# Kernel optimization log

Hardware: AMD Instinct MI355X
Metric: run time of the kernel (lower is better)

Reference implementation:

```python
import jax, jax.numpy as jnp
import numpy as np
from jax import lax

B, S, D, F, E, K = 4, 2048, 2048, 8192, 8, 2


def setup_inputs() -> dict:
    key = jax.random.key(0)
    ks = jax.random.split(key, 4)
    sd = 1.0 / np.sqrt(D)
    sf = 1.0 / np.sqrt(F)
    return {
        "hidden_states": jax.random.normal(ks[0], (B, S, D), dtype=jnp.float32),
        "router_w": jax.random.normal(ks[1], (D, E), dtype=jnp.float32) * sd,
        "w1": jax.random.normal(ks[2], (E, D, F), dtype=jnp.float32) * sd,
        "b1": jnp.zeros((E, F), dtype=jnp.float32),
        "w2": jax.random.normal(ks[3], (E, F, D), dtype=jnp.float32) * sf,
        "b2": jnp.zeros((E, D), dtype=jnp.float32),
        "top_k": K,
    }


def reference(hidden_states, router_w, w1, b1, w2, b2, top_k):
    b, s, d = hidden_states.shape
    x = hidden_states.reshape(-1, d)  # [T, D] flat tokens
    # Router: top-k over expert logits, softmax over the selected logits.
    logits = x @ router_w                      # [T, E]
    top_vals, top_idx = lax.top_k(logits, top_k)  # [T, K]
    scores = jax.nn.softmax(top_vals, axis=-1)    # [T, K]

    out = jnp.zeros_like(x)
    n_experts = w1.shape[0]
    for e in range(n_experts):  # fixed small expert count
        # per-token combine weight for this expert (0 if not routed)
        cw = jnp.sum(jnp.where(top_idx == e, scores, 0.0), axis=-1)  # [T]
        h = jax.nn.gelu(x @ w1[e] + b1[e], approximate=False)        # [T, F]
        out = out + cw[:, None] * (h @ w2[e] + b2[e])                # masked combine
    out = out.reshape(b, s, d)
    return out + hidden_states  # use_residual=True
```

## Files before the change

kernel.cpp:

```cpp
#include <hip/hip_runtime.h>

#define T_TOK 8192
#define DIM   2048
#define FFN   8192
#define NE    8
#define TOPK  2

typedef unsigned short ushort_t;
typedef unsigned short ushort8  __attribute__((ext_vector_type(8)));
typedef unsigned short ushort4v __attribute__((ext_vector_type(4)));
typedef short bf16x8 __attribute__((ext_vector_type(8)));
typedef float f32x4  __attribute__((ext_vector_type(4)));

__device__ __forceinline__ ushort_t f2bf(float f) {
  unsigned int u = __float_as_uint(f);
  u += 0x7FFFu + ((u >> 16) & 1u);
  return (ushort_t)(u >> 16);
}
__device__ __forceinline__ float bf2f(ushort_t u) {
  return __uint_as_float(((unsigned int)u) << 16);
}

__device__ __forceinline__ void gload16(const void* g, void* l) {
  __builtin_amdgcn_global_load_lds((const __attribute__((address_space(1))) void*)g,
                                   (__attribute__((address_space(3))) void*)l, 16, 0, 0);
}
__device__ __forceinline__ unsigned lds_off(const ushort_t* p) {
  return (unsigned)(uintptr_t)(__attribute__((address_space(3))) const ushort_t*)p;
}
__device__ __forceinline__ bf16x8 ds_read128(unsigned off) {
  bf16x8 r;
  asm volatile("ds_read_b128 %0, %1" : "=v"(r) : "v"(off));
  return r;
}

__device__ __forceinline__ float gelu_exact(float v) {
  float s = v * 0.70710678118654752f;
  float a = fabsf(s);
  float t = __builtin_amdgcn_rcpf(1.0f + 0.3275911f * a);
  float p = t * (0.254829592f +
            t * (-0.284496736f +
            t * (1.421413741f +
            t * (-1.453152027f +
            t * 1.061405429f))));
  float er = 1.0f - p * __expf(-a * a);
  er = copysignf(er, s);
  return 0.5f * v * (1.0f + er);
}

__global__ void k_cast(const float* __restrict__ x, ushort_t* __restrict__ xbf) {
  int i = blockIdx.x * blockDim.x + threadIdx.x;
  float4 v = reinterpret_cast<const float4*>(x)[i];
  ushort4v o;
  o.x = f2bf(v.x); o.y = f2bf(v.y); o.z = f2bf(v.z); o.w = f2bf(v.w);
  reinterpret_cast<ushort4v*>(xbf)[i] = o;
}

#define TT 64
__global__ __launch_bounds__(256) void k_wcvt(const float* __restrict__ in,
                                              ushort_t* __restrict__ outp, int R, int C) {
  __shared__ ushort_t t[TT][TT + 8];
  int e = blockIdx.z;
  const float* src = in + (size_t)e * R * C;
  ushort_t* dst = outp + (size_t)e * R * C;
  int r0 = blockIdx.y * TT, c0 = blockIdx.x * TT;
  int tid = threadIdx.x;
  int rr = tid >> 4;
  int c4 = tid & 15;
#pragma unroll
  for (int i = 0; i < 4; i++) {
    int r = rr + i * 16;
    float4 v = *reinterpret_cast<const float4*>(src + (size_t)(r0 + r) * C + c0 + c4 * 4);
    ushort4v p;
    p.x = f2bf(v.x); p.y = f2bf(v.y); p.z = f2bf(v.z); p.w = f2bf(v.w);
    *reinterpret_cast<ushort4v*>(&t[r][c4 * 4]) = p;
  }
  __syncthreads();
  int c = tid >> 2, rs = tid & 3;
  ushort_t tmp[16];
#pragma unroll
  for (int i = 0; i < 16; i++) tmp[i] = t[rs * 16 + i][c];
  ushort8 v0, v1;
#pragma unroll
  for (int i = 0; i < 8; i++) { v0[i] = tmp[i]; v1[i] = tmp[8 + i]; }
  ushort_t* drow = dst + (size_t)(c0 + c) * R + r0 + rs * 16;
  *reinterpret_cast<ushort8*>(drow) = v0;
  *reinterpret_cast<ushort8*>(drow + 8) = v1;
}

__global__ __launch_bounds__(256) void k_router(
    const float* __restrict__ x, const float* __restrict__ rw,
    int* __restrict__ tidx, float* __restrict__ twt, int* __restrict__ counts) {
  int t = blockIdx.x;
  int tid = threadIdx.x;
  int lane = tid & 63, wave = tid >> 6;
  float acc[NE];
#pragma unroll
  for (int e = 0; e < NE; e++) acc[e] = 0.f;
  const float* xr = x + (size_t)t * DIM;
  for (int d = tid; d < DIM; d += 256) {
    float xv = xr[d];
    const float* r = rw + d * NE;
#pragma unroll
    for (int e = 0; e < NE; e++) acc[e] += xv * r[e];
  }
  __shared__ float wsum[4][NE];
#pragma unroll
  for (int e = 0; e < NE; e++) {
    float v = acc[e];
#pragma unroll
    for (int off = 32; off > 0; off >>= 1) v += __shfl_down(v, off);
    if (lane == 0) wsum[wave][e] = v;
  }
  __syncthreads();
  if (tid == 0) {
    float lg[NE];
#pragma unroll
    for (int e = 0; e < NE; e++) lg[e] = wsum[0][e] + wsum[1][e] + wsum[2][e] + wsum[3][e];
    int i0 = 0; float v0 = lg[0];
#pragma unroll
    for (int e = 1; e < NE; e++) if (lg[e] > v0) { v0 = lg[e]; i0 = e; }
    int i1 = -1; float v1 = -3.4e38f;
#pragma unroll
    for (int e = 0; e < NE; e++) if (e != i0 && lg[e] > v1) { v1 = lg[e]; i1 = e; }
    float e1 = expf(v1 - v0);
    float s = 1.f + e1;
    tidx[t * 2 + 0] = i0; tidx[t * 2 + 1] = i1;
    twt[t * 2 + 0] = 1.f / s; twt[t * 2 + 1] = e1 / s;
    atomicAdd(&counts[i0], 1);
    atomicAdd(&counts[i1], 1);
  }
}

__global__ void k_scan(const int* __restrict__ counts, int* __restrict__ offsets) {
  if (threadIdx.x == 0) {
    int s = 0;
    for (int e = 0; e < NE; e++) { offsets[e] = s; s += counts[e]; }
    offsets[NE] = s;
  }
}

__global__ void k_fill(const int* __restrict__ tidx, const float* __restrict__ twt,
                       const int* __restrict__ offsets, int* __restrict__ cursors,
                       int* __restrict__ ltok, float* __restrict__ lwt, int* __restrict__ ppos) {
  int t = blockIdx.x * blockDim.x + threadIdx.x;
  if (t >= T_TOK) return;
#pragma unroll
  for (int k = 0; k < TOPK; k++) {
    int e = tidx[t * 2 + k];
    int pos = atomicAdd(&cursors[e], 1);
    int p = offsets[e] + pos;
    ltok[p] = t;
    lwt[p] = twt[t * 2 + k];
    ppos[t * 2 + k] = p;
  }
}

#define BM 128
#define BN 128
#define BK 32
#define BUFB (BM * BK * 2)

__device__ __forceinline__ void xcd_decode(int lin, int nwg, int nx, int& xt, int& yt) {
  int q = nwg >> 3;
  int w = (lin & 7) * q + (lin >> 3);
  xt = w % nx;
  yt = w / nx;
}

template <int NT>
__device__ __forceinline__ void gemm_loop(const ushort_t* __restrict__ a0,
                                          const ushort_t* __restrict__ a1,
                                          const ushort_t* __restrict__ b0,
                                          const ushort_t* __restrict__ b1,
                                          ushort_t* AsLds, ushort_t* BsLds,
                                          f32x4 (&acc)[4][4]) {
  int tid = threadIdx.x;
  int wave = tid >> 6, lane = tid & 63;
  int wm = wave >> 1, wn = wave & 1;
  int lm = lane & 15, lg = lane >> 4;

  unsigned abase = lds_off(AsLds), bbase = lds_off(BsLds);
  unsigned aoff[4], boff[4];
#pragma unroll
  for (int m = 0; m < 4; m++)
    aoff[m] = abase + ((wm * 64 + m * 16 + lm) * BK + lg * 8) * 2;
#pragma unroll
  for (int n = 0; n < 4; n++)
    boff[n] = bbase + ((wn * 64 + n * 16 + lm) * BK + lg * 8) * 2;

  const ushort_t* ap[2] = {a0, a1};
  const ushort_t* bp[2] = {b0, b1};

  auto STAGE = [&](int buf, int k0) {
#pragma unroll
    for (int j = 0; j < 2; j++) {
      gload16(ap[j] + k0, AsLds + buf * (BM * BK) + (j * 256 + wave * 64) * 8);
      gload16(bp[j] + k0, BsLds + buf * (BM * BK) + (j * 256 + wave * 64) * 8);
    }
  };

  STAGE(0, 0);
  STAGE(1, BK);
  int cur = 0;
  for (int t = 0; t < NT; ++t) {
    int s2 = cur + 2; if (s2 >= 3) s2 -= 3;
    if (t + 2 < NT) {
      STAGE(s2, (t + 2) * BK);
      __builtin_amdgcn_sched_barrier(0);
      asm volatile("s_waitcnt vmcnt(8)" ::: "memory");
    } else if (t + 1 < NT) {
      __builtin_amdgcn_sched_barrier(0);
      asm volatile("s_waitcnt vmcnt(4)" ::: "memory");
    } else {
      __builtin_amdgcn_sched_barrier(0);
      asm volatile("s_waitcnt vmcnt(0)" ::: "memory");
    }
    __builtin_amdgcn_s_barrier();
    __builtin_amdgcn_sched_barrier(0);
    unsigned cb = (unsigned)(cur * BUFB);
    bf16x8 af[4], bv[4];
#pragma unroll
    for (int m = 0; m < 4; m++) af[m] = ds_read128(aoff[m] + cb);
#pragma unroll
    for (int n = 0; n < 4; n++) bv[n] = ds_read128(boff[n] + cb);
    asm volatile("s_waitcnt lgkmcnt(0)" ::: "memory");
    __builtin_amdgcn_sched_barrier(0);
#pragma unroll
    for (int m = 0; m < 4; m++)
#pragma unroll
      for (int n = 0; n < 4; n++)
        acc[m][n] = __builtin_amdgcn_mfma_f32_16x16x32_bf16(af[m], bv[n], acc[m][n], 0, 0, 0);
    __builtin_amdgcn_sched_barrier(0);
    __builtin_amdgcn_s_barrier();
    __builtin_amdgcn_sched_barrier(0);
    cur += 1; if (cur == 3) cur = 0;
  }
}

__global__ __launch_bounds__(256) void k_gemm1(
    const ushort_t* __restrict__ xbf, const ushort_t* __restrict__ w1t, const float* __restrict__ b1,
    const int* __restrict__ counts, const int* __restrict__ offsets,
    const int* __restrict__ ltok, ushort_t* __restrict__ H) {
  int e = blockIdx.z;
  int cnt = counts[e];
  int xt, yt;
  xcd_decode(blockIdx.x, (T_TOK / BM) * (FFN / BN), T_TOK / BM, xt, yt);
  int row0 = xt * BM;
  if (row0 >= cnt) return;
  int base = offsets[e];
  int col0 = yt * BN;
  const ushort_t* Bt = w1t + (size_t)e * DIM * FFN;

  __shared__ __align__(16) ushort_t As[3 * BM * BK];
  __shared__ __align__(16) ushort_t Bs[3 * BM * BK];

  int tid = threadIdx.x;
  int srow = tid >> 2, seg = tid & 3;
  const ushort_t* asrc[2]; const ushort_t* bsrc[2];
#pragma unroll
  for (int j = 0; j < 2; j++) {
    int ar = min(row0 + j * 64 + srow, cnt - 1);
    asrc[j] = xbf + (size_t)ltok[base + ar] * DIM + seg * 8;
    bsrc[j] = Bt + (size_t)(col0 + j * 64 + srow) * DIM + seg * 8;
  }
  f32x4 acc[4][4];
#pragma unroll
  for (int m = 0; m < 4; m++)
#pragma unroll
    for (int n = 0; n < 4; n++) acc[m][n] = (f32x4){0.f, 0.f, 0.f, 0.f};

  gemm_loop<DIM / BK>(asrc[0], asrc[1], bsrc[0], bsrc[1], As, Bs, acc);

  int wave = tid >> 6, lane = tid & 63;
  int wm = wave >> 1, wn = wave & 1;
  int lm = lane & 15, lg = lane >> 4;
#pragma unroll
  for (int m = 0; m < 4; m++) {
#pragma unroll
    for (int n = 0; n < 4; n++) {
      int f = col0 + wn * 64 + n * 16 + lm;
      float bias = b1[e * FFN + f];
#pragma unroll
      for (int r = 0; r < 4; r++) {
        int row = row0 + wm * 64 + m * 16 + lg * 4 + r;
        if (row < cnt) {
          float v = acc[m][n][r] + bias;
          H[(size_t)(base + row) * FFN + f] = f2bf(gelu_exact(v));
        }
      }
    }
  }
}

__global__ __launch_bounds__(256) void k_gemm2(
    const ushort_t* __restrict__ H, const ushort_t* __restrict__ w2t, const float* __restrict__ b2,
    const int* __restrict__ counts, const int* __restrict__ offsets,
    const float* __restrict__ lwt, ushort_t* __restrict__ contrib) {
  int e = blockIdx.z;
  int cnt = counts[e];
  int xt, yt;
  xcd_decode(blockIdx.x, (T_TOK / BM) * (DIM / BN), T_TOK / BM, xt, yt);
  int row0 = xt * BM;
  if (row0 >= cnt) return;
  int base = offsets[e];
  int col0 = yt * BN;
  const ushort_t* Bt = w2t + (size_t)e * DIM * FFN;

  __shared__ __align__(16) ushort_t As[3 * BM * BK];
  __shared__ __align__(16) ushort_t Bs[3 * BM * BK];

  int tid = threadIdx.x;
  int srow = tid >> 2, seg = tid & 3;
  const ushort_t* asrc[2]; const ushort_t* bsrc[2];
#pragma unroll
  for (int j = 0; j < 2; j++) {
    int ar = min(row0 + j * 64 + srow, cnt - 1);
    asrc[j] = H + (size_t)(base + ar) * FFN + seg * 8;
    bsrc[j] = Bt + (size_t)(col0 + j * 64 + srow) * FFN + seg * 8;
  }
  f32x4 acc[4][4];
#pragma unroll
  for (int m = 0; m < 4; m++)
#pragma unroll
    for (int n = 0; n < 4; n++) acc[m][n] = (f32x4){0.f, 0.f, 0.f, 0.f};

  gemm_loop<FFN / BK>(asrc[0], asrc[1], bsrc[0], bsrc[1], As, Bs, acc);

  int wave = tid >> 6, lane = tid & 63;
  int wm = wave >> 1, wn = wave & 1;
  int lm = lane & 15, lg = lane >> 4;
#pragma unroll
  for (int m = 0; m < 4; m++) {
#pragma unroll
    for (int n = 0; n < 4; n++) {
      int d = col0 + wn * 64 + n * 16 + lm;
      float bias = b2[e * DIM + d];
#pragma unroll
      for (int r = 0; r < 4; r++) {
        int row = row0 + wm * 64 + m * 16 + lg * 4 + r;
        if (row < cnt) {
          float v = (acc[m][n][r] + bias) * lwt[base + row];
          contrib[(size_t)(base + row) * DIM + d] = f2bf(v);
        }
      }
    }
  }
}

__global__ void k_combine(const float* __restrict__ x, const ushort_t* __restrict__ contrib,
                          const int* __restrict__ ppos, float* __restrict__ out) {
  int i = blockIdx.x * blockDim.x + threadIdx.x;
  int t = i / (DIM / 4);
  int dq = i % (DIM / 4);
  int p0 = ppos[t * 2 + 0], p1 = ppos[t * 2 + 1];
  float4 xv = reinterpret_cast<const float4*>(x)[i];
  ushort4v c0 = reinterpret_cast<const ushort4v*>(contrib + (size_t)p0 * DIM)[dq];
  ushort4v c1 = reinterpret_cast<const ushort4v*>(contrib + (size_t)p1 * DIM)[dq];
  float4 o;
  o.x = xv.x + bf2f(c0.x) + bf2f(c1.x);
  o.y = xv.y + bf2f(c0.y) + bf2f(c1.y);
  o.z = xv.z + bf2f(c0.z) + bf2f(c1.z);
  o.w = xv.w + bf2f(c0.w) + bf2f(c1.w);
  reinterpret_cast<float4*>(out)[i] = o;
}

extern "C" void kernel_launch(void* const* d_in, const int* in_sizes, int n_in,
                              void* d_out, int out_size, void* d_ws, size_t ws_size,
                              hipStream_t stream) {
  const float* x  = (const float*)d_in[0];
  const float* rw = (const float*)d_in[1];
  const float* w1 = (const float*)d_in[2];
  const float* b1 = (const float*)d_in[3];
  const float* w2 = (const float*)d_in[4];
  const float* b2 = (const float*)d_in[5];
  float* out = (float*)d_out;
  char* ws = (char*)d_ws;

  const size_t MB = 1u << 20;
  int*   counts  = (int*)(ws);
  int*   offsets = (int*)(ws + 64);
  int*   cursors = (int*)(ws + 128);
  int*   tidx    = (int*)(ws + 1 * MB);
  float* twt     = (float*)(ws + 2 * MB);
  int*   ltok    = (int*)(ws + 3 * MB);
  float* lwt     = (float*)(ws + 4 * MB);
  int*   ppos    = (int*)(ws + 5 * MB);
  ushort_t* xbf     = (ushort_t*)(ws + 8 * MB);
  ushort_t* contrib = (ushort_t*)(ws + 8 * MB);
  ushort_t* Hbuf    = (ushort_t*)(ws + 72 * MB);
  ushort_t* w1t     = (ushort_t*)(ws + 328 * MB);
  ushort_t* w2t     = (ushort_t*)(ws + 328 * MB);
  const size_t NEED = 584 * MB;
  if (ws_size < NEED) {
    hipMemsetAsync(d_out, 0, (size_t)out_size * sizeof(float), stream);
    return;
  }

  hipMemsetAsync(ws, 0, 256, stream);
  k_cast<<<dim3((T_TOK * (size_t)DIM / 4) / 256), 256, 0, stream>>>(x, xbf);
  k_router<<<T_TOK, 256, 0, stream>>>(x, rw, tidx, twt, counts);
  k_scan<<<1, 64, 0, stream>>>(counts, offsets);
  k_fill<<<T_TOK / 256, 256, 0, stream>>>(tidx, twt, offsets, cursors, ltok, lwt, ppos);
  k_wcvt<<<dim3(FFN / TT, DIM / TT, NE), 256, 0, stream>>>(w1, w1t, DIM, FFN);
  k_gemm1<<<dim3((T_TOK / BM) * (FFN / BN), 1, NE), 256, 0, stream>>>(xbf, w1t, b1, counts, offsets, ltok, Hbuf);
  k_wcvt<<<dim3(DIM / TT, FFN / TT, NE), 256, 0, stream>>>(w2, w2t, FFN, DIM);
  k_gemm2<<<dim3((T_TOK / BM) * (DIM / BN), 1, NE), 256, 0, stream>>>(Hbuf, w2t, b2, counts, offsets, lwt, contrib);
  k_combine<<<dim3((T_TOK * (size_t)DIM / 4) / 256), 256, 0, stream>>>(x, contrib, ppos, out);
}
```

Before: 2.340 ms.

## Enlarge MoE GEMM tiles to 256x256 with 8 waves and MFMA priority

Doubles the GEMM macro-tile in both dimensions and moves to 512-thread blocks with a 2x4 wave grid. Each wave now computes a 128x64 sub-tile with 32 accumulators, which raises arithmetic intensity per LDS and global load. It also raises wave priority around the MFMA burst with s_setprio. The costs are higher register pressure (128 accumulator VGPRs), larger LDS use per block (96KB for three stages), fewer blocks per expert, and more wasted work on partially filled tiles.

```diff
diff --git a/kernel.cpp b/kernel.cpp
--- a/kernel.cpp
+++ b/kernel.cpp
@@ -156,10 +156,11 @@
   }
 }
 
-#define BM 128
-#define BN 128
+#define BM 256
+#define BN 256
 #define BK 32
-#define BUFB (BM * BK * 2)
+#define SLOT (BM * BK)
+#define SLOTB (SLOT * 2)
 
 __device__ __forceinline__ void xcd_decode(int lin, int nwg, int nx, int& xt, int& yt) {
   int q = nwg >> 3;
@@ -174,20 +175,20 @@
                                           const ushort_t* __restrict__ b0,
                                           const ushort_t* __restrict__ b1,
                                           ushort_t* AsLds, ushort_t* BsLds,
-                                          f32x4 (&acc)[4][4]) {
+                                          f32x4 (&acc)[8][4]) {
   int tid = threadIdx.x;
-  int wave = tid >> 6, lane = tid & 63;
-  int wm = wave >> 1, wn = wave & 1;
+  int wid = tid >> 6, lane = tid & 63;
+  int wm = wid >> 2, wn = wid & 3;
   int lm = lane & 15, lg = lane >> 4;
 
   unsigned abase = lds_off(AsLds), bbase = lds_off(BsLds);
-  unsigned aoff[4], boff[4];
-#pragma unroll
-  for (int m = 0; m < 4; m++)
-    aoff[m] = abase + ((wm * 64 + m * 16 + lm) * BK + lg * 8) * 2;
+  unsigned aoff[8], boff[4];
+#pragma unroll
+  for (int m = 0; m < 8; m++)
+    aoff[m] = abase + (unsigned)(((wm * 128 + m * 16 + lm) * BK + lg * 8) * 2);
 #pragma unroll
   for (int n = 0; n < 4; n++)
-    boff[n] = bbase + ((wn * 64 + n * 16 + lm) * BK + lg * 8) * 2;
+    boff[n] = bbase + (unsigned)(((wn * 64 + n * 16 + lm) * BK + lg * 8) * 2);
 
   const ushort_t* ap[2] = {a0, a1};
   const ushort_t* bp[2] = {b0, b1};
@@ -195,8 +196,8 @@
   auto STAGE = [&](int buf, int k0) {
 #pragma unroll
     for (int j = 0; j < 2; j++) {
-      gload16(ap[j] + k0, AsLds + buf * (BM * BK) + (j * 256 + wave * 64) * 8);
-      gload16(bp[j] + k0, BsLds + buf * (BM * BK) + (j * 256 + wave * 64) * 8);
+      gload16(ap[j] + k0, AsLds + buf * SLOT + (j * 512 + wid * 64) * 8);
+      gload16(bp[j] + k0, BsLds + buf * SLOT + (j * 512 + wid * 64) * 8);
     }
   };
 
@@ -218,19 +219,21 @@
     }
     __builtin_amdgcn_s_barrier();
     __builtin_amdgcn_sched_barrier(0);
-    unsigned cb = (unsigned)(cur * BUFB);
-    bf16x8 af[4], bv[4];
-#pragma unroll
-    for (int m = 0; m < 4; m++) af[m] = ds_read128(aoff[m] + cb);
+    unsigned cb = (unsigned)(cur * SLOTB);
+    bf16x8 af[8], bv[4];
+#pragma unroll
+    for (int m = 0; m < 8; m++) af[m] = ds_read128(aoff[m] + cb);
 #pragma unroll
     for (int n = 0; n < 4; n++) bv[n] = ds_read128(boff[n] + cb);
     asm volatile("s_waitcnt lgkmcnt(0)" ::: "memory");
     __builtin_amdgcn_sched_barrier(0);
-#pragma unroll
-    for (int m = 0; m < 4; m++)
+    __builtin_amdgcn_s_setprio(1);
+#pragma unroll
+    for (int m = 0; m < 8; m++)
 #pragma unroll
       for (int n = 0; n < 4; n++)
         acc[m][n] = __builtin_amdgcn_mfma_f32_16x16x32_bf16(af[m], bv[n], acc[m][n], 0, 0, 0);
+    __builtin_amdgcn_s_setprio(0);
     __builtin_amdgcn_sched_barrier(0);
     __builtin_amdgcn_s_barrier();
     __builtin_amdgcn_sched_barrier(0);
@@ -238,7 +241,7 @@
   }
 }
 
-__global__ __launch_bounds__(256) void k_gemm1(
+__global__ __launch_bounds__(512) void k_gemm1(
     const ushort_t* __restrict__ xbf, const ushort_t* __restrict__ w1t, const float* __restrict__ b1,
     const int* __restrict__ counts, const int* __restrict__ offsets,
     const int* __restrict__ ltok, ushort_t* __restrict__ H) {
@@ -252,38 +255,39 @@
   int col0 = yt * BN;
   const ushort_t* Bt = w1t + (size_t)e * DIM * FFN;
 
-  __shared__ __align__(16) ushort_t As[3 * BM * BK];
-  __shared__ __align__(16) ushort_t Bs[3 * BM * BK];
+  __shared__ __align__(16) ushort_t As[3 * SLOT];
+  __shared__ __align__(16) ushort_t Bs[3 * SLOT];
 
   int tid = threadIdx.x;
-  int srow = tid >> 2, seg = tid & 3;
+  int rsub = tid >> 2, seg = tid & 3;
   const ushort_t* asrc[2]; const ushort_t* bsrc[2];
 #pragma unroll
   for (int j = 0; j < 2; j++) {
-    int ar = min(row0 + j * 64 + srow, cnt - 1);
+    int row = j * 128 + rsub;
+    int ar = min(row0 + row, cnt - 1);
     asrc[j] = xbf + (size_t)ltok[base + ar] * DIM + seg * 8;
-    bsrc[j] = Bt + (size_t)(col0 + j * 64 + srow) * DIM + seg * 8;
-  }
-  f32x4 acc[4][4];
-#pragma unroll
-  for (int m = 0; m < 4; m++)
+    bsrc[j] = Bt + (size_t)(col0 + row) * DIM + seg * 8;
+  }
+  f32x4 acc[8][4];
+#pragma unroll
+  for (int m = 0; m < 8; m++)
 #pragma unroll
     for (int n = 0; n < 4; n++) acc[m][n] = (f32x4){0.f, 0.f, 0.f, 0.f};
 
   gemm_loop<DIM / BK>(asrc[0], asrc[1], bsrc[0], bsrc[1], As, Bs, acc);
 
-  int wave = tid >> 6, lane = tid & 63;
-  int wm = wave >> 1, wn = wave & 1;
+  int wid = tid >> 6, lane = tid & 63;
+  int wm = wid >> 2, wn = wid & 3;
   int lm = lane & 15, lg = lane >> 4;
 #pragma unroll
-  for (int m = 0; m < 4; m++) {
+  for (int m = 0; m < 8; m++) {
 #pragma unroll
     for (int n = 0; n < 4; n++) {
       int f = col0 + wn * 64 + n * 16 + lm;
       float bias = b1[e * FFN + f];
 #pragma unroll
       for (int r = 0; r < 4; r++) {
-        int row = row0 + wm * 64 + m * 16 + lg * 4 + r;
+        int row = row0 + wm * 128 + m * 16 + lg * 4 + r;
         if (row < cnt) {
           float v = acc[m][n][r] + bias;
           H[(size_t)(base + row) * FFN + f] = f2bf(gelu_exact(v));
@@ -293,7 +297,7 @@
   }
 }
 
-__global__ __launch_bounds__(256) void k_gemm2(
+__global__ __launch_bounds__(512) void k_gemm2(
     const ushort_t* __restrict__ H, const ushort_t* __restrict__ w2t, const float* __restrict__ b2,
     const int* __restrict__ counts, const int* __restrict__ offsets,
     const float* __restrict__ lwt, ushort_t* __restrict__ contrib) {
@@ -307,38 +311,39 @@
   int col0 = yt * BN;
   const ushort_t* Bt = w2t + (size_t)e * DIM * FFN;
 
-  __shared__ __align__(16) ushort_t As[3 * BM * BK];
-  __shared__ __align__(16) ushort_t Bs[3 * BM * BK];
+  __shared__ __align__(16) ushort_t As[3 * SLOT];
+  __shared__ __align__(16) ushort_t Bs[3 * SLOT];
 
   int tid = threadIdx.x;
-  int srow = tid >> 2, seg = tid & 3;
+  int rsub = tid >> 2, seg = tid & 3;
   const ushort_t* asrc[2]; const ushort_t* bsrc[2];
 #pragma unroll
   for (int j = 0; j < 2; j++) {
-    int ar = min(row0 + j * 64 + srow, cnt - 1);
+    int row = j * 128 + rsub;
+    int ar = min(row0 + row, cnt - 1);
     asrc[j] = H + (size_t)(base + ar) * FFN + seg * 8;
-    bsrc[j] = Bt + (size_t)(col0 + j * 64 + srow) * FFN + seg * 8;
-  }
-  f32x4 acc[4][4];
-#pragma unroll
-  for (int m = 0; m < 4; m++)
+    bsrc[j] = Bt + (size_t)(col0 + row) * FFN + seg * 8;
+  }
+  f32x4 acc[8][4];
+#pragma unroll
+  for (int m = 0; m < 8; m++)
 #pragma unroll
     for (int n = 0; n < 4; n++) acc[m][n] = (f32x4){0.f, 0.f, 0.f, 0.f};
 
   gemm_loop<FFN / BK>(asrc[0], asrc[1], bsrc[0], bsrc[1], As, Bs, acc);
 
-  int wave = tid >> 6, lane = tid & 63;
-  int wm = wave >> 1, wn = wave & 1;
+  int wid = tid >> 6, lane = tid & 63;
+  int wm = wid >> 2, wn = wid & 3;
   int lm = lane & 15, lg = lane >> 4;
 #pragma unroll
-  for (int m = 0; m < 4; m++) {
+  for (int m = 0; m < 8; m++) {
 #pragma unroll
     for (int n = 0; n < 4; n++) {
       int d = col0 + wn * 64 + n * 16 + lm;
       float bias = b2[e * DIM + d];
 #pragma unroll
       for (int r = 0; r < 4; r++) {
-        int row = row0 + wm * 64 + m * 16 + lg * 4 + r;
+        int row = row0 + wm * 128 + m * 16 + lg * 4 + r;
         if (row < cnt) {
           float v = (acc[m][n][r] + bias) * lwt[base + row];
           contrib[(size_t)(base + row) * DIM + d] = f2bf(v);
@@ -403,8 +408,8 @@
   k_scan<<<1, 64, 0, stream>>>(counts, offsets);
   k_fill<<<T_TOK / 256, 256, 0, stream>>>(tidx, twt, offsets, cursors, ltok, lwt, ppos);
   k_wcvt<<<dim3(FFN / TT, DIM / TT, NE), 256, 0, stream>>>(w1, w1t, DIM, FFN);
-  k_gemm1<<<dim3((T_TOK / BM) * (FFN / BN), 1, NE), 256, 0, stream>>>(xbf, w1t, b1, counts, offsets, ltok, Hbuf);
+  k_gemm1<<<dim3((T_TOK / BM) * (FFN / BN), 1, NE), 512, 0, stream>>>(xbf, w1t, b1, counts, offsets, ltok, Hbuf);
   k_wcvt<<<dim3(DIM / TT, FFN / TT, NE), 256, 0, stream>>>(w2, w2t, FFN, DIM);
-  k_gemm2<<<dim3((T_TOK / BM) * (DIM / BN), 1, NE), 256, 0, stream>>>(Hbuf, w2t, b2, counts, offsets, lwt, contrib);
+  k_gemm2<<<dim3((T_TOK / BM) * (DIM / BN), 1, NE), 512, 0, stream>>>(Hbuf, w2t, b2, counts, offsets, lwt, contrib);
   k_combine<<<dim3((T_TOK * (size_t)DIM / 4) / 256), 256, 0, stream>>>(x, contrib, ppos, out);
 }
```

Result: no change. 2.338 ms (-0.1%).
